# Kernel optimization log

Measured on AMD Instinct MI355X. Metric: run time of the kernel, lower is better.

## Reference

```python
import jax, jax.numpy as jnp
import numpy as np

RANGE_DISP = 32
IND_INPUT_VIEW = np.array([1, 9]) - 1  # 0-based indices of the two input views
TOTAL_VIEWS = 9                         # an_sparse + an_novel
FEAT_CH = 64


def conv2d(x, w, b):
    # x: (N, Cin, H, W), w: (Cout, Cin, kh, kw), SAME padding, stride 1
    y = jax.lax.conv_general_dilated(x, w, (1, 1), 'SAME',
                                     dimension_numbers=('NCHW', 'OIHW', 'NCHW'))
    return y + b[None, :, None, None]


def unfold_1xK(x, K):
    # torch.nn.functional.unfold(x, kernel_size=(1, K)) for x: (M, C, H, W)
    # -> (M, C, K, H*(W-K+1)), column index = h*(W-K+1) + w (row-major).
    M, C, H, W = x.shape
    out_w = W - K + 1
    cols = jnp.arange(out_w)[None, :] + jnp.arange(K)[:, None]  # (K, out_w)
    y = x[:, :, :, cols]             # (M, C, H, K, out_w)
    y = y.transpose(0, 1, 3, 2, 4)   # (M, C, K, H, out_w)
    return y.reshape(M, C, K, H * out_w)


def setup_inputs() -> dict:
    key = jax.random.key(0)
    ks = jax.random.split(key, 24)
    b, an_sparse, an_novel, rp = 2, 2, 7, 32
    K = RANGE_DISP
    ps = rp + K - 1  # 63

    def rn(k, shape, s=1.0):
        return jax.random.normal(k, shape, dtype=jnp.float32) * s

    W = 0.05  # weight init scale
    return {
        'lf_sparse':        rn(ks[0], (b, an_sparse, rp, ps)),
        'flow_sparse':      rn(ks[1], (b, an_sparse, rp, ps)),
        'warped_lf_sparse': rn(ks[2], (b, an_sparse, rp, ps)),
        'patch_left':       rn(ks[3], (b, an_novel, rp, rp)),
        'patch_right':      rn(ks[4], (b, an_novel, rp, rp)),
        # FlowRefNet: 3 -> 64 -> 64 -> 64, 3x3 convs, SAME
        'fr_w1': rn(ks[5], (FEAT_CH, 3, 3, 3), W), 'fr_b1': jnp.zeros((FEAT_CH,), jnp.float32),
        'fr_w2': rn(ks[6], (FEAT_CH, FEAT_CH, 3, 3), W), 'fr_b2': jnp.zeros((FEAT_CH,), jnp.float32),
        'fr_w3': rn(ks[7], (FEAT_CH, FEAT_CH, 3, 3), W), 'fr_b3': jnp.zeros((FEAT_CH,), jnp.float32),
        # MlpNet: per-disparity MLP 67 -> 64 -> 64 -> 1 (weight head) + conf head 64 -> 1
        'mlp_w1': rn(ks[8], (67, 64), W), 'mlp_b1': jnp.zeros((64,), jnp.float32),
        'mlp_w2': rn(ks[9], (64, 64), W), 'mlp_b2': jnp.zeros((64,), jnp.float32),
        'mlp_w3': rn(ks[10], (64, 1), W), 'mlp_b3': jnp.zeros((1,), jnp.float32),
        'conf_w': rn(ks[11], (64, 1), W), 'conf_b': jnp.zeros((1,), jnp.float32),
        # ViewRefNet: 3 -> 64 -> 64 -> 1 convs, residual on novel patch
        'vr_w1': rn(ks[12], (FEAT_CH, 3, 3, 3), W), 'vr_b1': jnp.zeros((FEAT_CH,), jnp.float32),
        'vr_w2': rn(ks[13], (FEAT_CH, FEAT_CH, 3, 3), W), 'vr_b2': jnp.zeros((FEAT_CH,), jnp.float32),
        'vr_w3': rn(ks[14], (1, FEAT_CH, 3, 3), W), 'vr_b3': jnp.zeros((1,), jnp.float32),
    }


def reference(lf_sparse, flow_sparse, warped_lf_sparse, patch_left, patch_right,
              fr_w1, fr_b1, fr_w2, fr_b2, fr_w3, fr_b3,
              mlp_w1, mlp_b1, mlp_w2, mlp_b2, mlp_w3, mlp_b3, conf_w, conf_b,
              vr_w1, vr_b1, vr_w2, vr_b2, vr_w3, vr_b3):
    b, an_sparse, rp, ps = lf_sparse.shape
    an_novel = patch_left.shape[1]
    K = RANGE_DISP
    N = rp * rp

    lf = lf_sparse.reshape(b * an_sparse, 1, rp, ps)
    fl = flow_sparse.reshape(b * an_sparse, 1, rp, ps)
    wp = warped_lf_sparse.reshape(b * an_sparse, 1, rp, ps)

    # FlowRefNet: flow-feature extraction
    h = jax.nn.relu(conv2d(jnp.concatenate([fl, lf, wp], axis=1), fr_w1, fr_b1))
    h = jax.nn.relu(conv2d(h, fr_w2, fr_b2))
    feat = jax.nn.relu(conv2d(h, fr_w3, fr_b3))  # (b*as, 64, rp, ps)

    # angular code: input-view index minus novel-view index
    ind_novel = np.delete(np.arange(TOTAL_VIEWS), IND_INPUT_VIEW)
    ang = jnp.asarray(IND_INPUT_VIEW[None, :] - ind_novel[:, None], dtype=lf.dtype)  # (an, as)
    spatial = (jnp.arange(K) - K // 2).astype(lf.dtype)  # (K,)

    # EPI windows via unfold(kernel=(1, K))
    flow_unf = unfold_1xK(fl, K)[:, 0]  # (b*as, K, N)
    feat_unf = unfold_1xK(feat, K)      # (b*as, 64, K, N)

    sh = (b, an_novel, an_sparse)
    f_flow = jnp.broadcast_to(flow_unf.reshape(b, 1, an_sparse, 1, K, N),  sh + (1, K, N))
    f_feat = jnp.broadcast_to(feat_unf.reshape(b, 1, an_sparse, FEAT_CH, K, N), sh + (FEAT_CH, K, N))
    f_spat = jnp.broadcast_to(spatial.reshape(1, 1, 1, 1, K, 1),           sh + (1, K, N))
    f_ang  = jnp.broadcast_to(ang.reshape(1, an_novel, an_sparse, 1, 1, 1), sh + (1, K, N))
    features = jnp.concatenate([f_flow, f_feat, f_spat, f_ang], axis=3)  # (b, an, as, 67, K, N)
    # -> (b*an*as*N, K, 67) matching permute(0,3,2,1).reshape in torch
    features = features.transpose(0, 1, 2, 5, 4, 3).reshape(-1, K, 67)

    # MlpNet: per-disparity weight + per-sample confidence
    h1 = jax.nn.relu(features @ mlp_w1 + mlp_b1)
    h2 = jax.nn.relu(h1 @ mlp_w2 + mlp_b2)          # (M2, K, 64)
    weight = (h2 @ mlp_w3 + mlp_b3)[..., 0]         # (M2, K)
    conf = (h2.mean(axis=1) @ conf_w + conf_b)[..., 0]  # (M2,)

    weight = jax.nn.softmax(weight.reshape(b, an_novel, an_sparse, N, K), axis=-1)
    confs = jax.nn.softmax(conf.reshape(b, an_novel, an_sparse, N), axis=2)

    # disparity-weighted combination over EPI windows
    epi = unfold_1xK(lf, K)[:, 0].reshape(b, an_sparse, K, N)
    nv = jnp.einsum('bskn,bvsnk->bvsn', epi, weight)   # (b, an, as, N)
    novel = (nv * confs).sum(axis=2)                   # (b, an, N)

    # ViewRefNet: residual refinement
    pn = novel.reshape(b * an_novel, 1, rp, rp)
    pl = patch_left.reshape(b * an_novel, 1, rp, rp)
    pr = patch_right.reshape(b * an_novel, 1, rp, rp)
    g = jax.nn.relu(conv2d(jnp.concatenate([pn, pl, pr], axis=1), vr_w1, vr_b1))
    g = jax.nn.relu(conv2d(g, vr_w2, vr_b2))
    res = conv2d(g, vr_w3, vr_b3)
    out = pn + res
    return out.reshape(b, an_novel, rp, rp)
```

## Files before the change

kernel.cpp:

```cpp
#include <hip/hip_runtime.h>

typedef unsigned short u16;
typedef unsigned int u32;
typedef __bf16 bf16x8 __attribute__((ext_vector_type(8)));
typedef float f32x4 __attribute__((ext_vector_type(4)));
typedef u16 u16x8 __attribute__((ext_vector_type(8)));

__device__ __forceinline__ u16 f2bf(float f) {
    __bf16 h = (__bf16)f;
    return __builtin_bit_cast(u16, h);
}
__device__ __forceinline__ float bf2f(u16 u) {
    unsigned int x = ((unsigned int)u) << 16;
    return __builtin_bit_cast(float, x);
}

union FragU { u16x8 u; bf16x8 v; };

constexpr size_t WB2F  = 0;
constexpr size_t WB3F  = 18432;
constexpr size_t WBV2  = 36864;
constexpr size_t W1T   = 55296;
constexpr size_t W2T   = 57344;
constexpr size_t X1    = 59392;
constexpr size_t X2    = 317440;
constexpr size_t FEATBF= 575488;
constexpr size_t NVOFF = 833536;
constexpr size_t CFOFF = 862208;

__global__ __launch_bounds__(256) void conv1feat_kernel(
    const float* __restrict__ in0, const float* __restrict__ in1,
    const float* __restrict__ in2,
    const float* __restrict__ wts, const float* __restrict__ bias,
    u16* __restrict__ out,
    const float* __restrict__ frw2, const float* __restrict__ frw3,
    const float* __restrict__ vrw2,
    const float* __restrict__ mw1, const float* __restrict__ mw2,
    u16* __restrict__ wb2, u16* __restrict__ wb3, u16* __restrict__ wbv,
    u16* __restrict__ w1t, u16* __restrict__ w2t)
{
    constexpr int W = 63, NPX = 2016, H = 32;
    const int t = threadIdx.x;
    if (blockIdx.z == 4) {
        const int tid = (blockIdx.y * 8 + blockIdx.x) * 256 + t;
        for (int i = tid; i < 36864; i += 16384) {
            int tap = i >> 12, och = (i >> 6) & 63, cin = i & 63;
            size_t s = (size_t)och * 576 + cin * 9 + tap;
            wb2[i] = f2bf(frw2[s]);
            wb3[i] = f2bf(frw3[s]);
            wbv[i] = f2bf(vrw2[s]);
        }
        for (int i = tid; i < 4096; i += 16384) {
            int col = i >> 6, r = i & 63;
            w1t[i] = f2bf(mw1[(1 + r) * 64 + col]);
            w2t[i] = f2bf(mw2[r * 64 + col]);
        }
        return;
    }
    const int px = blockIdx.y * 256 + t;
    const int m = blockIdx.z;
    const int og = blockIdx.x;
    if (px >= NPX) return;
    const int y = px / W, x = px - y * W;

    float acc[8];
#pragma unroll
    for (int oc = 0; oc < 8; ++oc) acc[oc] = bias[og * 8 + oc];

#pragma unroll
    for (int cin = 0; cin < 3; ++cin) {
        const float* ip = (cin == 0 ? in0 : (cin == 1 ? in1 : in2)) + (size_t)m * NPX;
        float tap[9];
#pragma unroll
        for (int dy = 0; dy < 3; ++dy) {
            int yy = y + dy - 1;
            bool ry = (yy >= 0) && (yy < H);
#pragma unroll
            for (int dx = 0; dx < 3; ++dx) {
                int xx = x + dx - 1;
                tap[dy * 3 + dx] = (ry && xx >= 0 && xx < W) ? ip[yy * W + xx] : 0.f;
            }
        }
#pragma unroll
        for (int oc = 0; oc < 8; ++oc) {
            const float* wr = wts + (size_t)(og * 8 + oc) * 27 + cin * 9;
#pragma unroll
            for (int j = 0; j < 9; ++j) acc[oc] = fmaf(tap[j], wr[j], acc[oc]);
        }
    }
    u16x8 pk;
#pragma unroll
    for (int oc = 0; oc < 8; ++oc) pk[oc] = f2bf(fmaxf(acc[oc], 0.f));
    *(u16x8*)(out + ((size_t)m * NPX + px) * 64 + og * 8) = pk;
}

template<int W, int NPX, int NT>
__global__ __launch_bounds__(256) void convmfma_kernel(
    const u16* __restrict__ in, const u16* __restrict__ wbf,
    const float* __restrict__ bias, u16* __restrict__ out)
{
    constexpr int H = 32;
    const int t = threadIdx.x;
    const int base = blockIdx.x * 64;
    const int ochb = blockIdx.y * (NT * 16);
    const int m = blockIdx.z;
    const int w = t >> 6, lane = t & 63, q = lane >> 4, l15 = lane & 15;

    const u16* im = in + (size_t)m * NPX * 64;
    const int pxA = base + w * 16 + l15;
    const int yA = pxA / W, xA = pxA - yA * W;
    const bool pxok = (pxA < NPX);

    f32x4 acc[NT];
#pragma unroll
    for (int nt = 0; nt < NT; ++nt) acc[nt] = f32x4{0.f, 0.f, 0.f, 0.f};

#pragma unroll
    for (int tap = 0; tap < 9; ++tap) {
        const int dy = tap / 3 - 1, dx = tap % 3 - 1;
        const bool valid = pxok && (yA + dy >= 0) && (yA + dy < H)
                                && (xA + dx >= 0) && (xA + dx < W);
        const u16* ap = im + (size_t)(pxA + dy * W + dx) * 64;
        FragU a0, a1;
        if (valid) {
            a0 = *(const FragU*)(ap + q * 8);
            a1 = *(const FragU*)(ap + 32 + q * 8);
        } else {
#pragma unroll
            for (int jj = 0; jj < 8; ++jj) { a0.u[jj] = 0; a1.u[jj] = 0; }
        }
#pragma unroll
        for (int nt = 0; nt < NT; ++nt) {
            const u16* bp = wbf + tap * 4096 + (ochb + nt * 16 + l15) * 64;
            FragU b0 = *(const FragU*)(bp + q * 8);
            FragU b1 = *(const FragU*)(bp + 32 + q * 8);
            acc[nt] = __builtin_amdgcn_mfma_f32_16x16x32_bf16(a0.v, b0.v, acc[nt], 0, 0, 0);
            acc[nt] = __builtin_amdgcn_mfma_f32_16x16x32_bf16(a1.v, b1.v, acc[nt], 0, 0, 0);
        }
    }

#pragma unroll
    for (int nt = 0; nt < NT; ++nt) {
        const float bb = bias[ochb + nt * 16 + l15];
#pragma unroll
        for (int e = 0; e < 4; ++e) {
            int pxs = base + w * 16 + q * 4 + e;
            if (pxs < NPX)
                out[((size_t)m * NPX + pxs) * 64 + ochb + nt * 16 + l15] =
                    f2bf(fmaxf(acc[nt][e] + bb, 0.f));
        }
    }
}

__global__ __launch_bounds__(256, 2) void mlp_mfma_kernel(
    const float* __restrict__ lf, const float* __restrict__ flow,
    const u16* __restrict__ feat,
    const u16* __restrict__ w1t, const u16* __restrict__ w2t,
    const float* __restrict__ w1, const float* __restrict__ b1,
    const float* __restrict__ b2,
    const float* __restrict__ w3, const float* __restrict__ b3g,
    const float* __restrict__ cw, const float* __restrict__ cbg,
    float* __restrict__ nv_out, float* __restrict__ cf_out)
{
    constexpr int SBS = 72;
    __shared__ __align__(16) float s_vec[7 * 64];
    __shared__ __align__(16) float s_flow[256];
    __shared__ __align__(16) float s_epi[256];
    __shared__ __align__(16) u16 s_base[256 * SBS];

    const int t = threadIdx.x;
    const int blk = blockIdx.x;
    const int bs = blk >> 7;
    const int n0 = (blk & 127) * 8;
    const int b = bs >> 1, s = bs & 1;
    const int w = t >> 6, lane = t & 63, q = lane >> 4, l15 = lane & 15;

    if (t < 64) {
        s_vec[t]       = b1[t];
        s_vec[64 + t]  = b2[t];
        s_vec[128 + t] = w3[t];
        s_vec[192 + t] = cw[t];
        s_vec[256 + t] = w1[t];
        s_vec[320 + t] = w1[65 * 64 + t];
        s_vec[384 + t] = w1[66 * 64 + t];
    }
    {
        int nl = t >> 5, k = t & 31;
        int n = n0 + nl;
        int a = (bs * 32 + (n >> 5)) * 63 + (n & 31) + k;
        s_flow[t] = flow[a];
        s_epi[t]  = lf[a];
    }
    __syncthreads();

    const float b3s = b3g[0];
    const float cbs = cbg[0];

    FragU w1b[2][4];
#pragma unroll
    for (int ks = 0; ks < 2; ++ks)
#pragma unroll
        for (int nt = 0; nt < 4; ++nt)
            w1b[ks][nt] = *(const FragU*)(w1t + (nt * 16 + l15) * 64 + ks * 32 + q * 8);

    float w1r0pl[4], w1r65pl[4], b1pl[4];
#pragma unroll
    for (int nt = 0; nt < 4; ++nt) {
        int j1 = nt * 16 + l15;
        w1r0pl[nt]  = s_vec[256 + j1];
        w1r65pl[nt] = s_vec[320 + j1];
        b1pl[nt]    = s_vec[j1];
    }

#pragma unroll
    for (int mt = 0; mt < 4; ++mt) {
        const int rbase = w * 64 + mt * 16;
        FragU af[2];
        {
            int r = rbase + l15;
            int n = n0 + (r >> 5);
            int pos = (n >> 5) * 63 + (n & 31) + (r & 31);
            const u16* fp = feat + ((size_t)bs * 2016 + pos) * 64;
            af[0] = *(const FragU*)(fp + q * 8);
            af[1] = *(const FragU*)(fp + 32 + q * 8);
        }
        f32x4 flow4 = *(const f32x4*)(s_flow + rbase + q * 4);
#pragma unroll
        for (int nt = 0; nt < 4; ++nt) {
            f32x4 d = {0.f, 0.f, 0.f, 0.f};
            d = __builtin_amdgcn_mfma_f32_16x16x32_bf16(af[0].v, w1b[0][nt].v, d, 0, 0, 0);
            d = __builtin_amdgcn_mfma_f32_16x16x32_bf16(af[1].v, w1b[1][nt].v, d, 0, 0, 0);
#pragma unroll
            for (int e = 0; e < 4; ++e) {
                int r = rbase + q * 4 + e;
                int k = r & 31;
                float val = d[e] + flow4[e] * w1r0pl[nt]
                          + (float)(k - 16) * w1r65pl[nt] + b1pl[nt];
                s_base[r * SBS + nt * 16 + l15] = f2bf(val);
            }
        }
    }
    __syncthreads();

    FragU w2a[4][2];
#pragma unroll
    for (int mt = 0; mt < 4; ++mt)
#pragma unroll
        for (int ks = 0; ks < 2; ++ks)
            w2a[mt][ks] = *(const FragU*)(w2t + (mt * 16 + l15) * 64 + ks * 32 + q * 8);

    float w66pl[2][8];
#pragma unroll
    for (int ks = 0; ks < 2; ++ks)
#pragma unroll
        for (int jj = 0; jj < 8; ++jj)
            w66pl[ks][jj] = s_vec[384 + ks * 32 + q * 8 + jj];

    float b2pl[4][4], w3pl[4][4], cwpl[4][4];
#pragma unroll
    for (int mt = 0; mt < 4; ++mt)
#pragma unroll
        for (int e = 0; e < 4; ++e) {
            b2pl[mt][e] = s_vec[64 + mt * 16 + q * 4 + e];
            w3pl[mt][e] = s_vec[128 + mt * 16 + q * 4 + e];
            cwpl[mt][e] = s_vec[192 + mt * 16 + q * 4 + e];
        }
    float epi_pl[4];
#pragma unroll
    for (int nt = 0; nt < 4; ++nt) epi_pl[nt] = s_epi[w * 64 + nt * 16 + l15];

    for (int v = 0; v < 7; ++v) {
        float ang = (s == 0) ? -(float)(v + 1) : (float)(7 - v);
        f32x4 acc[4][4];
#pragma unroll
        for (int nt = 0; nt < 4; ++nt) {
            FragU bfr[2];
#pragma unroll
            for (int ks = 0; ks < 2; ++ks) {
                const u16x8 raw = *(const u16x8*)(s_base + (w * 64 + nt * 16 + l15) * SBS + ks * 32 + q * 8);
#pragma unroll
                for (int jj = 0; jj < 8; ++jj) {
                    float xv = bf2f(raw[jj]);
                    float hv = fmaxf(xv + ang * w66pl[ks][jj], 0.f);
                    bfr[ks].u[jj] = f2bf(hv);
                }
            }
#pragma unroll
            for (int mt = 0; mt < 4; ++mt) {
                f32x4 d = {0.f, 0.f, 0.f, 0.f};
                d = __builtin_amdgcn_mfma_f32_16x16x32_bf16(w2a[mt][0].v, bfr[0].v, d, 0, 0, 0);
                d = __builtin_amdgcn_mfma_f32_16x16x32_bf16(w2a[mt][1].v, bfr[1].v, d, 0, 0, 0);
                acc[mt][nt] = d;
            }
        }
        float wl[4], cfl[4];
#pragma unroll
        for (int nt = 0; nt < 4; ++nt) {
            float wls = 0.f, cfs = 0.f;
#pragma unroll
            for (int mt = 0; mt < 4; ++mt)
#pragma unroll
                for (int e = 0; e < 4; ++e) {
                    float h2 = fmaxf(acc[mt][nt][e] + b2pl[mt][e], 0.f);
                    wls += h2 * w3pl[mt][e];
                    cfs += h2 * cwpl[mt][e];
                }
            wls += __shfl_xor(wls, 16); wls += __shfl_xor(wls, 32);
            cfs += __shfl_xor(cfs, 16); cfs += __shfl_xor(cfs, 32);
            wl[nt]  = wls + b3s;
            cfl[nt] = cfs;
        }
#pragma unroll
        for (int ni = 0; ni < 2; ++ni) {
            float a0 = wl[ni * 2], a1 = wl[ni * 2 + 1];
            float mx = fmaxf(a0, a1);
#pragma unroll
            for (int msk = 1; msk <= 8; msk <<= 1) mx = fmaxf(mx, __shfl_xor(mx, msk));
            float e0 = __expf(a0 - mx), e1 = __expf(a1 - mx);
            float ssum = e0 + e1;
            float nvp = e0 * epi_pl[ni * 2] + e1 * epi_pl[ni * 2 + 1];
            float cfp = cfl[ni * 2] + cfl[ni * 2 + 1];
#pragma unroll
            for (int msk = 1; msk <= 8; msk <<= 1) {
                ssum += __shfl_xor(ssum, msk);
                nvp  += __shfl_xor(nvp, msk);
                cfp  += __shfl_xor(cfp, msk);
            }
            if (lane == 0) {
                int n = n0 + w * 2 + ni;
                size_t idx = ((size_t)(b * 7 + v) * 2 + s) * 1024 + n;
                nv_out[idx] = nvp / ssum;
                cf_out[idx] = cfp * (1.f / 32.f) + cbs;
            }
        }
    }
}

__global__ __launch_bounds__(512, 4) void refine_kernel(
    const float* __restrict__ nv, const float* __restrict__ cf,
    const float* __restrict__ pl, const float* __restrict__ pr,
    const float* __restrict__ vrw1, const float* __restrict__ vrb1,
    const u16* __restrict__ wbv, const float* __restrict__ vrb2,
    const float* __restrict__ vrw3, const float* __restrict__ vrb3,
    float* __restrict__ out)
{
    __shared__ __align__(16) float pn_s[10][32];
    __shared__ __align__(16) float pls[10][32];
    __shared__ __align__(16) float prs[10][32];
    __shared__ __align__(16) float sw3[576];
    __shared__ __align__(16) u16 g1_s[8 * 32 * 64];
    __shared__ __align__(16) u16 g2_s[6 * 32 * 64];

    const int t = threadIdx.x;
    const int pt = blockIdx.x;
    const int m  = blockIdx.y;
    const int y0 = pt * 4;

    if (t < 320) {
        int rr = t >> 5, col = t & 31;
        int gy = y0 - 3 + rr;
        float vv = 0.f, vl = 0.f, vr = 0.f;
        if (gy >= 0 && gy < 32) {
            int n = gy * 32 + col;
            size_t i0 = ((size_t)m * 2) * 1024 + n;
            size_t i1 = i0 + 1024;
            float c0 = cf[i0], c1 = cf[i1];
            float mx = fmaxf(c0, c1);
            float e0 = __expf(c0 - mx), e1 = __expf(c1 - mx);
            vv = (e0 * nv[i0] + e1 * nv[i1]) / (e0 + e1);
            vl = pl[(size_t)m * 1024 + n];
            vr = pr[(size_t)m * 1024 + n];
        }
        pn_s[rr][col] = vv;
        pls[rr][col] = vl;
        prs[rr][col] = vr;
    }
    for (int i = t; i < 576; i += 512) sw3[i] = vrw3[i];
    __syncthreads();

    {
        const int wv = __builtin_amdgcn_readfirstlane(t >> 6);
        const int lane = t & 63;
        const int oh = wv & 1;
        const int px_i = (wv >> 1) * 64 + lane;
        const int lr0 = px_i >> 5;
        const int x = px_i & 31;
        const int gy = y0 - 2 + lr0;
        const bool inimg = (gy >= 0) && (gy < 32);

        float tap0[9], tap1[9], tap2[9];
#pragma unroll
        for (int dy = 0; dy < 3; ++dy) {
            const int prow = lr0 + dy;
#pragma unroll
            for (int dx = 0; dx < 3; ++dx) {
                int xx = x + dx - 1;
                bool rx = (xx >= 0) && (xx < 32);
                tap0[dy * 3 + dx] = rx ? pn_s[prow][xx] : 0.f;
                tap1[dy * 3 + dx] = rx ? pls[prow][xx] : 0.f;
                tap2[dy * 3 + dx] = rx ? prs[prow][xx] : 0.f;
            }
        }
#pragma unroll
        for (int jg = 0; jg < 4; ++jg) {
            u16x8 pk;
#pragma unroll
            for (int e = 0; e < 8; ++e) {
                const int o = oh * 32 + jg * 8 + e;
                const float* wr = vrw1 + (size_t)o * 27;
                float acc = vrb1[o];
#pragma unroll
                for (int j = 0; j < 9; ++j) acc = fmaf(tap0[j], wr[j], acc);
#pragma unroll
                for (int j = 0; j < 9; ++j) acc = fmaf(tap1[j], wr[9 + j], acc);
#pragma unroll
                for (int j = 0; j < 9; ++j) acc = fmaf(tap2[j], wr[18 + j], acc);
                pk[e] = f2bf(inimg ? fmaxf(acc, 0.f) : 0.f);
            }
            int byte = (px_i * 128 + oh * 64 + jg * 16) ^ ((px_i & 7) << 4);
            *(u16x8*)((char*)g1_s + byte) = pk;
        }
    }
    __syncthreads();

    {
        const int w = t >> 6, lane = t & 63, q = lane >> 4, l15 = lane & 15;
        const int ocht = w & 3, base = ocht * 16;
        const int wg = w >> 2;

        f32x4 acc[6];
#pragma unroll
        for (int i = 0; i < 6; ++i) acc[i] = f32x4{0.f, 0.f, 0.f, 0.f};

#pragma unroll
        for (int tap = 0; tap < 9; ++tap) {
            const int dy = tap / 3 - 1, dx = tap % 3 - 1;
            const u16* bp = wbv + tap * 4096 + (base + l15) * 64;
            FragU b0 = *(const FragU*)(bp + q * 8);
            FragU b1 = *(const FragU*)(bp + 32 + q * 8);
#pragma unroll
            for (int i = 0; i < 6; ++i) {
                const int p = (wg + 2 * i) * 16 + l15;
                const int xx = (p & 31) + dx;
                const int p1 = p + (dy + 1) * 32 + dx;
                FragU a0, a1;
                if (xx >= 0 && xx < 32) {
                    int byte = (p1 * 128 + q * 16) ^ ((p1 & 7) << 4);
                    a0 = *(const FragU*)((const char*)g1_s + byte);
                    byte = (p1 * 128 + 64 + q * 16) ^ ((p1 & 7) << 4);
                    a1 = *(const FragU*)((const char*)g1_s + byte);
                } else {
#pragma unroll
                    for (int jj = 0; jj < 8; ++jj) { a0.u[jj] = 0; a1.u[jj] = 0; }
                }
                acc[i] = __builtin_amdgcn_mfma_f32_16x16x32_bf16(a0.v, b0.v, acc[i], 0, 0, 0);
                acc[i] = __builtin_amdgcn_mfma_f32_16x16x32_bf16(a1.v, b1.v, acc[i], 0, 0, 0);
            }
        }

        const float bb = vrb2[base + l15];
#pragma unroll
        for (int i = 0; i < 6; ++i) {
#pragma unroll
            for (int e = 0; e < 4; ++e) {
                int p = (wg + 2 * i) * 16 + q * 4 + e;
                int gy2 = y0 - 1 + (p >> 5);
                float vv = (gy2 >= 0 && gy2 < 32) ? fmaxf(acc[i][e] + bb, 0.f) : 0.f;
                int byte = (p * 128 + (base + l15) * 2) ^ ((p & 7) << 4);
                *(u16*)((char*)g2_s + byte) = f2bf(vv);
            }
        }
    }
    __syncthreads();

    {
        const int px_i = t >> 2;
        const int part = t & 3;
        const int ly = px_i >> 5;
        const int x  = px_i & 31;

        float a = 0.f;
#pragma unroll
        for (int dy = 0; dy < 3; ++dy) {
#pragma unroll
            for (int dx = 0; dx < 3; ++dx) {
                int xx = x + dx - 1;
                if (xx < 0 || xx >= 32) continue;
                int p2 = px_i + dy * 32 + dx - 1;
                const int tap = dy * 3 + dx;
                int byte0 = (p2 * 128 + part * 32) ^ ((p2 & 7) << 4);
                int byte1 = (p2 * 128 + part * 32 + 16) ^ ((p2 & 7) << 4);
                u16x8 r0 = *(const u16x8*)((const char*)g2_s + byte0);
                u16x8 r1 = *(const u16x8*)((const char*)g2_s + byte1);
#pragma unroll
                for (int e = 0; e < 8; ++e) {
                    a = fmaf(bf2f(r0[e]), sw3[(part * 16 + e) * 9 + tap], a);
                    a = fmaf(bf2f(r1[e]), sw3[(part * 16 + 8 + e) * 9 + tap], a);
                }
            }
        }
        a += __shfl_xor(a, 1);
        a += __shfl_xor(a, 2);
        if (part == 0) {
            int gy = y0 + ly;
            out[(size_t)m * 1024 + gy * 32 + x] = pn_s[ly + 3][x] + a + vrb3[0];
        }
    }
}

extern "C" void kernel_launch(void* const* d_in, const int* in_sizes, int n_in,
                              void* d_out, int out_size, void* d_ws, size_t ws_size,
                              hipStream_t stream) {
    const float* lf   = (const float*)d_in[0];
    const float* flow = (const float*)d_in[1];
    const float* wp   = (const float*)d_in[2];
    const float* pl   = (const float*)d_in[3];
    const float* pr   = (const float*)d_in[4];
    float* ws = (float*)d_ws;

    conv1feat_kernel<<<dim3(8, 8, 5), 256, 0, stream>>>(
        flow, lf, wp, (const float*)d_in[5], (const float*)d_in[6],
        (u16*)(ws + X1),
        (const float*)d_in[7], (const float*)d_in[9], (const float*)d_in[21],
        (const float*)d_in[11], (const float*)d_in[13],
        (u16*)(ws + WB2F), (u16*)(ws + WB3F), (u16*)(ws + WBV2),
        (u16*)(ws + W1T), (u16*)(ws + W2T));

    convmfma_kernel<63, 2016, 1><<<dim3(32, 4, 4), 256, 0, stream>>>(
        (const u16*)(ws + X1), (const u16*)(ws + WB2F), (const float*)d_in[8],
        (u16*)(ws + X2));
    convmfma_kernel<63, 2016, 1><<<dim3(32, 4, 4), 256, 0, stream>>>(
        (const u16*)(ws + X2), (const u16*)(ws + WB3F), (const float*)d_in[10],
        (u16*)(ws + FEATBF));

    mlp_mfma_kernel<<<512, 256, 0, stream>>>(
        lf, flow, (const u16*)(ws + FEATBF),
        (const u16*)(ws + W1T), (const u16*)(ws + W2T),
        (const float*)d_in[11], (const float*)d_in[12],
        (const float*)d_in[14],
        (const float*)d_in[15], (const float*)d_in[16],
        (const float*)d_in[17], (const float*)d_in[18],
        ws + NVOFF, ws + CFOFF);

    refine_kernel<<<dim3(8, 14), 512, 0, stream>>>(
        ws + NVOFF, ws + CFOFF, pl, pr,
        (const float*)d_in[19], (const float*)d_in[20],
        (const u16*)(ws + WBV2), (const float*)d_in[22],
        (const float*)d_in[23], (const float*)d_in[24],
        (float*)d_out);
}
```

Measured before the change: 179.8 us.

## Fuse FlowRefNet conv2 and conv3 into one kernel with halo rows in LDS

Replaces the two separate MFMA conv launches with a single kernel per output row. Each block computes conv2 for three rows (the output row plus a halo row on each side), stores them in a swizzled LDS buffer, then computes conv3 for the central row from LDS. This removes one launch and the global round trip of the intermediate activation. In exchange it recomputes conv2 halo rows about three times, and it uses fewer, larger blocks (128 blocks of 512 threads) than before.

After: 192.9 us. +7.3%, slower.

```diff
diff --git a/kernel.cpp b/kernel.cpp
--- a/kernel.cpp
+++ b/kernel.cpp
@@ -23,7 +23,6 @@
 constexpr size_t W1T   = 55296;
 constexpr size_t W2T   = 57344;
 constexpr size_t X1    = 59392;
-constexpr size_t X2    = 317440;
 constexpr size_t FEATBF= 575488;
 constexpr size_t NVOFF = 833536;
 constexpr size_t CFOFF = 862208;
@@ -94,60 +93,104 @@
     *(u16x8*)(out + ((size_t)m * NPX + px) * 64 + og * 8) = pk;
 }
 
-template<int W, int NPX, int NT>
-__global__ __launch_bounds__(256) void convmfma_kernel(
-    const u16* __restrict__ in, const u16* __restrict__ wbf,
-    const float* __restrict__ bias, u16* __restrict__ out)
+__global__ __launch_bounds__(512) void feat23_kernel(
+    const u16* __restrict__ x1, const u16* __restrict__ wb2,
+    const float* __restrict__ frb2, const u16* __restrict__ wb3,
+    const float* __restrict__ frb3, u16* __restrict__ featout)
 {
-    constexpr int H = 32;
+    __shared__ __align__(16) u16 g2_s[192 * 64];
+
     const int t = threadIdx.x;
-    const int base = blockIdx.x * 64;
-    const int ochb = blockIdx.y * (NT * 16);
-    const int m = blockIdx.z;
+    const int y0 = blockIdx.x;
+    const int m  = blockIdx.y;
     const int w = t >> 6, lane = t & 63, q = lane >> 4, l15 = lane & 15;
-
-    const u16* im = in + (size_t)m * NPX * 64;
-    const int pxA = base + w * 16 + l15;
-    const int yA = pxA / W, xA = pxA - yA * W;
-    const bool pxok = (pxA < NPX);
-
-    f32x4 acc[NT];
-#pragma unroll
-    for (int nt = 0; nt < NT; ++nt) acc[nt] = f32x4{0.f, 0.f, 0.f, 0.f};
-
-#pragma unroll
-    for (int tap = 0; tap < 9; ++tap) {
-        const int dy = tap / 3 - 1, dx = tap % 3 - 1;
-        const bool valid = pxok && (yA + dy >= 0) && (yA + dy < H)
-                                && (xA + dx >= 0) && (xA + dx < W);
-        const u16* ap = im + (size_t)(pxA + dy * W + dx) * 64;
-        FragU a0, a1;
-        if (valid) {
-            a0 = *(const FragU*)(ap + q * 8);
-            a1 = *(const FragU*)(ap + 32 + q * 8);
-        } else {
-#pragma unroll
-            for (int jj = 0; jj < 8; ++jj) { a0.u[jj] = 0; a1.u[jj] = 0; }
-        }
-#pragma unroll
-        for (int nt = 0; nt < NT; ++nt) {
-            const u16* bp = wbf + tap * 4096 + (ochb + nt * 16 + l15) * 64;
+    const u16* im = x1 + (size_t)m * 2016 * 64;
+
+#pragma unroll
+    for (int i = 0; i < 6; ++i) {
+        const int task = w + i * 8;
+        const int tile = task >> 2, qb = task & 3;
+        const int och  = qb * 16 + l15;
+        const int pl2  = tile * 16 + l15;
+        const int ly   = pl2 / 63;
+        const int x    = pl2 - ly * 63;
+        const int gy   = y0 - 1 + ly;
+        const bool pok = (pl2 < 189) && (gy >= 0) && (gy < 32);
+        const int pg   = gy * 63 + x;
+
+        f32x4 acc = f32x4{0.f, 0.f, 0.f, 0.f};
+#pragma unroll
+        for (int tap = 0; tap < 9; ++tap) {
+            const int dy = tap / 3 - 1, dx = tap % 3 - 1;
+            const bool valid = pok && (gy + dy >= 0) && (gy + dy < 32)
+                                   && (x + dx >= 0) && (x + dx < 63);
+            const u16* ap = im + (size_t)(pg + dy * 63 + dx) * 64;
+            FragU a0, a1;
+            if (valid) {
+                a0 = *(const FragU*)(ap + q * 8);
+                a1 = *(const FragU*)(ap + 32 + q * 8);
+            } else {
+#pragma unroll
+                for (int jj = 0; jj < 8; ++jj) { a0.u[jj] = 0; a1.u[jj] = 0; }
+            }
+            const u16* bp = wb2 + tap * 4096 + och * 64;
             FragU b0 = *(const FragU*)(bp + q * 8);
             FragU b1 = *(const FragU*)(bp + 32 + q * 8);
-            acc[nt] = __builtin_amdgcn_mfma_f32_16x16x32_bf16(a0.v, b0.v, acc[nt], 0, 0, 0);
-            acc[nt] = __builtin_amdgcn_mfma_f32_16x16x32_bf16(a1.v, b1.v, acc[nt], 0, 0, 0);
-        }
-    }
-
-#pragma unroll
-    for (int nt = 0; nt < NT; ++nt) {
-        const float bb = bias[ochb + nt * 16 + l15];
+            acc = __builtin_amdgcn_mfma_f32_16x16x32_bf16(a0.v, b0.v, acc, 0, 0, 0);
+            acc = __builtin_amdgcn_mfma_f32_16x16x32_bf16(a1.v, b1.v, acc, 0, 0, 0);
+        }
+
+        const float bb = frb2[och];
 #pragma unroll
         for (int e = 0; e < 4; ++e) {
-            int pxs = base + w * 16 + q * 4 + e;
-            if (pxs < NPX)
-                out[((size_t)m * NPX + pxs) * 64 + ochb + nt * 16 + l15] =
-                    f2bf(fmaxf(acc[nt][e] + bb, 0.f));
+            const int po  = tile * 16 + q * 4 + e;
+            const int lyo = po / 63;
+            const int gyo = y0 - 1 + lyo;
+            float vv = (po < 189 && gyo >= 0 && gyo < 32) ? fmaxf(acc[e] + bb, 0.f) : 0.f;
+            int byte = (po * 128 + och * 2) ^ ((po & 7) << 4);
+            *(u16*)((char*)g2_s + byte) = f2bf(vv);
+        }
+    }
+    __syncthreads();
+
+#pragma unroll
+    for (int i = 0; i < 2; ++i) {
+        const int task = w + i * 8;
+        const int tile = task >> 2, qb = task & 3;
+        const int och  = qb * 16 + l15;
+        const int pl3r = tile * 16 + l15;
+        const int x    = (pl3r < 63) ? pl3r : 0;
+
+        f32x4 acc = f32x4{0.f, 0.f, 0.f, 0.f};
+#pragma unroll
+        for (int tap = 0; tap < 9; ++tap) {
+            const int dy = tap / 3 - 1, dx = tap % 3 - 1;
+            const int xx = x + dx;
+            FragU a0, a1;
+            if (xx >= 0 && xx < 63) {
+                const int pl2s = (1 + dy) * 63 + xx;
+                int byte = (pl2s * 128 + q * 16) ^ ((pl2s & 7) << 4);
+                a0 = *(const FragU*)((const char*)g2_s + byte);
+                byte = (pl2s * 128 + 64 + q * 16) ^ ((pl2s & 7) << 4);
+                a1 = *(const FragU*)((const char*)g2_s + byte);
+            } else {
+#pragma unroll
+                for (int jj = 0; jj < 8; ++jj) { a0.u[jj] = 0; a1.u[jj] = 0; }
+            }
+            const u16* bp = wb3 + tap * 4096 + och * 64;
+            FragU b0 = *(const FragU*)(bp + q * 8);
+            FragU b1 = *(const FragU*)(bp + 32 + q * 8);
+            acc = __builtin_amdgcn_mfma_f32_16x16x32_bf16(a0.v, b0.v, acc, 0, 0, 0);
+            acc = __builtin_amdgcn_mfma_f32_16x16x32_bf16(a1.v, b1.v, acc, 0, 0, 0);
+        }
+
+        const float bb = frb3[och];
+#pragma unroll
+        for (int e = 0; e < 4; ++e) {
+            const int po = tile * 16 + q * 4 + e;
+            if (po < 63)
+                featout[((size_t)m * 2016 + y0 * 63 + po) * 64 + och] =
+                    f2bf(fmaxf(acc[e] + bb, 0.f));
         }
     }
 }
@@ -526,11 +569,9 @@
         (u16*)(ws + WB2F), (u16*)(ws + WB3F), (u16*)(ws + WBV2),
         (u16*)(ws + W1T), (u16*)(ws + W2T));
 
-    convmfma_kernel<63, 2016, 1><<<dim3(32, 4, 4), 256, 0, stream>>>(
+    feat23_kernel<<<dim3(32, 4), 512, 0, stream>>>(
         (const u16*)(ws + X1), (const u16*)(ws + WB2F), (const float*)d_in[8],
-        (u16*)(ws + X2));
-    convmfma_kernel<63, 2016, 1><<<dim3(32, 4, 4), 256, 0, stream>>>(
-        (const u16*)(ws + X2), (const u16*)(ws + WB3F), (const float*)d_in[10],
+        (const u16*)(ws + WB3F), (const float*)d_in[10],
         (u16*)(ws + FEATBF));
 
     mlp_mfma_kernel<<<512, 256, 0, stream>>>(
```
